# Kernel tuning notes

Hardware: AMD Instinct MI355X
Metric: run time of the kernel (lower is better)

Reference implementation:

```python
import jax, jax.numpy as jnp
import numpy as np

N = 50000   # nodes
E = 800000  # edges (avg degree 16)
F_IN = 128
H = 128
L = 4
LN_EPS = 1e-5


def setup_inputs() -> dict:
    key = jax.random.key(0)
    ks = jax.random.split(key, 4)
    x = jax.random.normal(ks[0], (N, F_IN), dtype=jnp.float32)
    edge_index = jax.random.randint(ks[1], (2, E), 0, N)
    conv_w = jax.random.normal(ks[2], (L, F_IN, H), dtype=jnp.float32) * 0.05
    conv_b = jnp.zeros((L, H), dtype=jnp.float32)
    ln_g = jnp.ones((L, H), dtype=jnp.float32)
    ln_b = jnp.zeros((L, H), dtype=jnp.float32)
    head_w = jax.random.normal(ks[3], (H, 1), dtype=jnp.float32) * 0.05
    head_b = jnp.zeros((1,), dtype=jnp.float32)
    return {"x": x, "edge_index": edge_index, "conv_w": conv_w, "conv_b": conv_b,
            "ln_g": ln_g, "ln_b": ln_b, "head_w": head_w, "head_b": head_b}


def _layer_norm(h, g, b):
    mu = jnp.mean(h, axis=-1, keepdims=True)
    var = jnp.mean(jnp.square(h - mu), axis=-1, keepdims=True)
    return (h - mu) * jax.lax.rsqrt(var + LN_EPS) * g + b


def _gcn_conv(h, W, b, src, dst, inv_sqrt_deg, inv_deg):
    # PyG GCNConv: self-loops + symmetric normalization D^-1/2 (A+I) D^-1/2, then bias.
    hw = h @ W  # (N, H)
    norm = inv_sqrt_deg[src] * inv_sqrt_deg[dst]  # (E,)
    msg = hw[src] * norm[:, None]  # gather + edgewise scale
    agg = jax.ops.segment_sum(msg, dst, num_segments=N)  # scatter-add
    agg = agg + hw * inv_deg[:, None]  # self-loop term (norm = 1/deg)
    return agg + b


def reference(x, edge_index, conv_w, conv_b, ln_g, ln_b, head_w, head_b):
    src, dst = edge_index[0], edge_index[1]
    # degree on target nodes, including self-loop
    deg = jax.ops.segment_sum(jnp.ones((E,), x.dtype), dst, num_segments=N) + 1.0
    inv_sqrt_deg = jax.lax.rsqrt(deg)
    inv_deg = 1.0 / deg
    h = x
    for i in range(L):
        h = _gcn_conv(h, conv_w[i], conv_b[i], src, dst, inv_sqrt_deg, inv_deg)
        h = _layer_norm(h, ln_g[i], ln_b[i])
        if i != L - 1:
            h = jax.nn.gelu(h, approximate=False)
            # dropout is identity in eval mode
    scores = (h @ head_w + head_b).squeeze(-1)  # (N,)
    return scores, h
```

## Files before the change

kernel.cpp:

```cpp
#include <hip/hip_runtime.h>
#include <math.h>

#define N_NODES 50000
#define N_EDGES 800000
#define HDIM 128
#define NLAYERS 4
#define LN_EPS 1e-5f

typedef __attribute__((ext_vector_type(8))) short short8;
typedef __attribute__((ext_vector_type(4))) float floatx4;

__device__ __forceinline__ ushort f2bf(float x) {
    unsigned b = __float_as_uint(x);
    unsigned r = b + 0x7fffu + ((b >> 16) & 1u);
    return (ushort)(r >> 16);
}
__device__ __forceinline__ float2 bf2f2(unsigned u) {
    return make_float2(__uint_as_float(u << 16), __uint_as_float(u & 0xffff0000u));
}


__global__ void deg_count_kernel(const int* __restrict__ dst, int* __restrict__ degcnt) {
    int e = blockIdx.x * blockDim.x + threadIdx.x;
    if (e < N_EDGES) atomicAdd(&degcnt[dst[e]], 1);
}

__global__ void scan1_kernel(const int* __restrict__ degcnt, int* __restrict__ partial,
                             int* __restrict__ blocksum) {
    __shared__ int buf[256];
    int tid = threadIdx.x;
    int i = blockIdx.x * 256 + tid;
    int v = (i < N_NODES) ? degcnt[i] : 0;
    buf[tid] = v;
    __syncthreads();
    for (int off = 1; off < 256; off <<= 1) {
        int t = (tid >= off) ? buf[tid - off] : 0;
        __syncthreads();
        buf[tid] += t;
        __syncthreads();
    }
    if (i < N_NODES) partial[i] = buf[tid] - v;
    if (tid == 255) blocksum[blockIdx.x] = buf[255];
}

__global__ void scan2_kernel(int* __restrict__ blocksum, int nblk) {
    __shared__ int buf[256];
    int tid = threadIdx.x;
    int v = (tid < nblk) ? blocksum[tid] : 0;
    buf[tid] = v;
    __syncthreads();
    for (int off = 1; off < 256; off <<= 1) {
        int t = (tid >= off) ? buf[tid - off] : 0;
        __syncthreads();
        buf[tid] += t;
        __syncthreads();
    }
    if (tid < nblk) blocksum[tid] = buf[tid] - v;
}

__global__ void scan3_kernel(const int* __restrict__ degcnt, const int* __restrict__ partial,
                             const int* __restrict__ blocksum, int* __restrict__ offs,
                             int* __restrict__ cursor, float* __restrict__ isd,
                             float* __restrict__ ind) {
    int i = blockIdx.x * blockDim.x + threadIdx.x;
    if (i < N_NODES) {
        int o = partial[i] + blocksum[i >> 8];
        offs[i] = o;
        cursor[i] = o;
        float d = (float)degcnt[i] + 1.0f;
        isd[i] = rsqrtf(d);
        ind[i] = 1.0f / d;
        if (i == 0) offs[N_NODES] = N_EDGES;
    }
}

__global__ void fill_kernel(const int* __restrict__ src, const int* __restrict__ dst,
                            const float* __restrict__ isd, int* __restrict__ cursor,
                            int* __restrict__ csr_src, float* __restrict__ csr_w) {
    int e = blockIdx.x * blockDim.x + threadIdx.x;
    if (e < N_EDGES) {
        int s = src[e], d = dst[e];
        int p = atomicAdd(&cursor[d], 1);
        csr_src[p] = s;
        csr_w[p] = isd[s] * isd[d];
    }
}

__global__ __launch_bounds__(256) void bprep_kernel(const float* __restrict__ W,
                                                    ushort* __restrict__ bfrag) {
    int idx = blockIdx.x * 256 + threadIdx.x;
    if (idx >= NLAYERS * 4 * 8 * 64) return;
    int lane = idx & 63;
    int t = (idx >> 6) & 7;
    int s = (idx >> 9) & 3;
    int l = idx >> 11;
    int n = t * 16 + (lane & 15);
    int kb = s * 32 + (lane >> 4) * 8;
    const float* Wl = W + (size_t)l * HDIM * HDIM;
    union { uint4 q; ushort u[8]; } o;
#pragma unroll
    for (int j = 0; j < 8; ++j) o.u[j] = f2bf(Wl[(size_t)(kb + j) * HDIM + n]);
    *(uint4*)&bfrag[(size_t)idx * 8] = o.q;
}

template <bool A_FP32>
__global__ __launch_bounds__(256) void gemm_mfma_kernel(const void* __restrict__ Av,
                                                        const ushort* __restrict__ bfrag,
                                                        ushort* __restrict__ out) {
    int wave = threadIdx.x >> 6, lane = threadIdx.x & 63;
    int quad = lane >> 4, mrow = lane & 15;
    int rowBase = blockIdx.x * 64 + wave * 16;
    int arow = rowBase + mrow;
    bool aok = arow < N_NODES;

    floatx4 acc[8];
#pragma unroll
    for (int t = 0; t < 8; ++t) acc[t] = (floatx4)0.f;

#pragma unroll
    for (int s = 0; s < 4; ++s) {
        union { short8 v; ushort u[8]; } af;
        if (A_FP32) {
            const float* A = (const float*)Av;
            if (aok) {
                const float* p = &A[(size_t)arow * HDIM + s * 32 + quad * 8];
#pragma unroll
                for (int j = 0; j < 8; ++j) af.u[j] = f2bf(p[j]);
            } else {
#pragma unroll
                for (int j = 0; j < 8; ++j) af.u[j] = 0;
            }
        } else {
            const ushort* A = (const ushort*)Av;
            if (aok) {
                af.v = *(const short8*)&A[(size_t)arow * HDIM + s * 32 + quad * 8];
            } else {
#pragma unroll
                for (int j = 0; j < 8; ++j) af.u[j] = 0;
            }
        }
#pragma unroll
        for (int t = 0; t < 8; ++t) {
            short8 bf = *(const short8*)&bfrag[(size_t)(((s * 8 + t) * 64) + lane) * 8];
            acc[t] = __builtin_amdgcn_mfma_f32_16x16x32_bf16(af.v, bf, acc[t], 0, 0, 0);
        }
    }
#pragma unroll
    for (int t = 0; t < 8; ++t) {
#pragma unroll
        for (int r = 0; r < 4; ++r) {
            int row = rowBase + quad * 4 + r;
            if (row < N_NODES) out[(size_t)row * HDIM + t * 16 + mrow] = f2bf(acc[t][r]);
        }
    }
}

__global__ __launch_bounds__(256) void agg_ln_kernel(
    const unsigned* __restrict__ hwu, const int* __restrict__ offs,
    const int* __restrict__ csr_src, const float* __restrict__ csr_w,
    const float* __restrict__ ind, const float* __restrict__ conv_b,
    const float* __restrict__ ln_g, const float* __restrict__ ln_b,
    unsigned* __restrict__ hout_bf, float* __restrict__ hout_f32,
    const float* __restrict__ head_w, const float* __restrict__ head_b,
    float* __restrict__ scores, int final_layer) {
    int wave = threadIdx.x >> 6;
    int lane = threadIdx.x & 63;
    int n = blockIdx.x * 4 + wave;
    if (n >= N_NODES) return;
    int c = lane * 2;

    float2 hv = bf2f2(hwu[(size_t)n * 64 + lane]);
    float idn = ind[n];
    float2 cb = *(const float2*)&conv_b[c];
    float ax = fmaf(hv.x, idn, cb.x);
    float ay = fmaf(hv.y, idn, cb.y);

    int rs = offs[n], re = offs[n + 1];
    for (int base = rs; base < re; base += 64) {
        int m = re - base;
        if (m > 64) m = 64;
        int sj = 0;
        float wj = 0.f;
        if (lane < m) { sj = csr_src[base + lane]; wj = csr_w[base + lane]; }
        int j = 0;
        for (; j + 4 <= m; j += 4) {
            int s0 = __shfl(sj, j + 0), s1 = __shfl(sj, j + 1);
            int s2 = __shfl(sj, j + 2), s3 = __shfl(sj, j + 3);
            float w0 = __shfl(wj, j + 0), w1 = __shfl(wj, j + 1);
            float w2 = __shfl(wj, j + 2), w3 = __shfl(wj, j + 3);
            unsigned u0 = hwu[(size_t)s0 * 64 + lane];
            unsigned u1 = hwu[(size_t)s1 * 64 + lane];
            unsigned u2 = hwu[(size_t)s2 * 64 + lane];
            unsigned u3 = hwu[(size_t)s3 * 64 + lane];
            float2 v0 = bf2f2(u0), v1 = bf2f2(u1), v2 = bf2f2(u2), v3 = bf2f2(u3);
            ax = fmaf(v0.x, w0, ax); ay = fmaf(v0.y, w0, ay);
            ax = fmaf(v1.x, w1, ax); ay = fmaf(v1.y, w1, ay);
            ax = fmaf(v2.x, w2, ax); ay = fmaf(v2.y, w2, ay);
            ax = fmaf(v3.x, w3, ax); ay = fmaf(v3.y, w3, ay);
        }
        for (; j < m; ++j) {
            int s = __shfl(sj, j);
            float w = __shfl(wj, j);
            float2 v = bf2f2(hwu[(size_t)s * 64 + lane]);
            ax = fmaf(v.x, w, ax);
            ay = fmaf(v.y, w, ay);
        }
    }

    float sum = ax + ay;
#pragma unroll
    for (int o = 32; o; o >>= 1) sum += __shfl_xor(sum, o);
    float mu = sum * (1.0f / HDIM);
    float dx = ax - mu, dy = ay - mu;
    float vs = dx * dx + dy * dy;
#pragma unroll
    for (int o = 32; o; o >>= 1) vs += __shfl_xor(vs, o);
    float rstd = rsqrtf(vs * (1.0f / HDIM) + LN_EPS);
    float2 g = *(const float2*)&ln_g[c];
    float2 b = *(const float2*)&ln_b[c];
    float yx = fmaf(dx * rstd, g.x, b.x);
    float yy = fmaf(dy * rstd, g.y, b.y);

    if (!final_layer) {
        yx = 0.5f * yx * (1.0f + erff(yx * 0.70710678118654752f));
        yy = 0.5f * yy * (1.0f + erff(yy * 0.70710678118654752f));
        hout_bf[(size_t)n * 64 + lane] = (unsigned)f2bf(yx) | ((unsigned)f2bf(yy) << 16);
    } else {
        *(float2*)&hout_f32[(size_t)n * HDIM + c] = make_float2(yx, yy);
        float2 hwv = *(const float2*)&head_w[c];
        float p = yx * hwv.x + yy * hwv.y;
#pragma unroll
        for (int o = 32; o; o >>= 1) p += __shfl_xor(p, o);
        if (lane == 0) scores[n] = p + head_b[0];
    }
}


extern "C" void kernel_launch(void* const* d_in, const int* in_sizes, int n_in,
                              void* d_out, int out_size, void* d_ws, size_t ws_size,
                              hipStream_t stream) {
    const float* x      = (const float*)d_in[0];
    const int*   eidx   = (const int*)d_in[1];
    const float* conv_w = (const float*)d_in[2];
    const float* conv_b = (const float*)d_in[3];
    const float* ln_g   = (const float*)d_in[4];
    const float* ln_b   = (const float*)d_in[5];
    const float* head_w = (const float*)d_in[6];
    const float* head_b = (const float*)d_in[7];
    float* out = (float*)d_out;

    const int* src = eidx;
    const int* dst = eidx + N_EDGES;

    char* ws = (char*)d_ws;
    size_t o = 0;
    auto alloc = [&](size_t elems) {
        void* p = ws + o * 4;
        o += (elems + 15) & ~(size_t)15;
        return p;
    };
    int*      degcnt   = (int*)alloc(N_NODES);
    float*    isd      = (float*)alloc(N_NODES);
    float*    ind      = (float*)alloc(N_NODES);
    int*      offs     = (int*)alloc(N_NODES + 1);
    int*      cursor   = (int*)alloc(N_NODES);
    int*      partial  = (int*)alloc(N_NODES);
    int*      blocksum = (int*)alloc(256);
    int*      csr_src  = (int*)alloc(N_EDGES);
    float*    csr_w    = (float*)alloc(N_EDGES);
    ushort*   bfrag    = (ushort*)alloc(NLAYERS * 4 * 8 * 64 * 8 / 2);
    unsigned* hw       = (unsigned*)alloc((size_t)N_NODES * 64);
    unsigned* hbuf     = (unsigned*)alloc((size_t)N_NODES * 64);

    hipMemsetAsync(degcnt, 0, N_NODES * sizeof(int), stream);
    deg_count_kernel<<<(N_EDGES + 255) / 256, 256, 0, stream>>>(dst, degcnt);
    int nblk = (N_NODES + 255) / 256;
    scan1_kernel<<<nblk, 256, 0, stream>>>(degcnt, partial, blocksum);
    scan2_kernel<<<1, 256, 0, stream>>>(blocksum, nblk);
    scan3_kernel<<<nblk, 256, 0, stream>>>(degcnt, partial, blocksum, offs, cursor, isd, ind);
    fill_kernel<<<(N_EDGES + 255) / 256, 256, 0, stream>>>(src, dst, isd, cursor, csr_src, csr_w);
    bprep_kernel<<<(NLAYERS * 4 * 8 * 64 + 255) / 256, 256, 0, stream>>>(conv_w, bfrag);

    const void* hin = (const void*)x;
    for (int l = 0; l < NLAYERS; ++l) {
        const ushort* bl = bfrag + (size_t)l * 4 * 8 * 64 * 8;
        if (l == 0)
            gemm_mfma_kernel<true><<<(N_NODES + 63) / 64, 256, 0, stream>>>(hin, bl, (ushort*)hw);
        else
            gemm_mfma_kernel<false><<<(N_NODES + 63) / 64, 256, 0, stream>>>(hin, bl, (ushort*)hw);
        int fin = (l == NLAYERS - 1) ? 1 : 0;
        agg_ln_kernel<<<(N_NODES + 3) / 4, 256, 0, stream>>>(
            hw, offs, csr_src, csr_w, ind,
            conv_b + (size_t)l * HDIM, ln_g + (size_t)l * HDIM, ln_b + (size_t)l * HDIM,
            hbuf, out + N_NODES, head_w, head_b, out, fin);
        hin = (const void*)hbuf;
    }
}
```

Measured before the change: 403.6 us.

## Compact CSR to 16-bit indices, atomic wave-level allocation, compute edge weights on the fly

Replaces the three-kernel prefix scan with a single kernel that does a wave-level scan and claims each wave's offset range with one atomic, so segments are no longer in node order. The CSR stores only 16-bit source indices, which is valid because there are fewer than 65536 nodes, and drops the per-edge float weight. The aggregation kernel looks up isd[src] per edge and applies isd[dst] once per node. The gather loop is unrolled to 8, with padded lanes carrying weight zero. This cuts CSR memory traffic and kernel launches, at the cost of an extra isd gather per edge and wasted padded loads for low-degree nodes.

```diff
diff --git a/kernel.cpp b/kernel.cpp
--- a/kernel.cpp
+++ b/kernel.cpp
@@ -25,64 +25,40 @@
     if (e < N_EDGES) atomicAdd(&degcnt[dst[e]], 1);
 }
 
-__global__ void scan1_kernel(const int* __restrict__ degcnt, int* __restrict__ partial,
-                             int* __restrict__ blocksum) {
-    __shared__ int buf[256];
-    int tid = threadIdx.x;
-    int i = blockIdx.x * 256 + tid;
-    int v = (i < N_NODES) ? degcnt[i] : 0;
-    buf[tid] = v;
-    __syncthreads();
-    for (int off = 1; off < 256; off <<= 1) {
-        int t = (tid >= off) ? buf[tid - off] : 0;
-        __syncthreads();
-        buf[tid] += t;
-        __syncthreads();
-    }
-    if (i < N_NODES) partial[i] = buf[tid] - v;
-    if (tid == 255) blocksum[blockIdx.x] = buf[255];
-}
-
-__global__ void scan2_kernel(int* __restrict__ blocksum, int nblk) {
-    __shared__ int buf[256];
-    int tid = threadIdx.x;
-    int v = (tid < nblk) ? blocksum[tid] : 0;
-    buf[tid] = v;
-    __syncthreads();
-    for (int off = 1; off < 256; off <<= 1) {
-        int t = (tid >= off) ? buf[tid - off] : 0;
-        __syncthreads();
-        buf[tid] += t;
-        __syncthreads();
-    }
-    if (tid < nblk) blocksum[tid] = buf[tid] - v;
-}
-
-__global__ void scan3_kernel(const int* __restrict__ degcnt, const int* __restrict__ partial,
-                             const int* __restrict__ blocksum, int* __restrict__ offs,
-                             int* __restrict__ cursor, float* __restrict__ isd,
-                             float* __restrict__ ind) {
-    int i = blockIdx.x * blockDim.x + threadIdx.x;
+__global__ __launch_bounds__(256) void alloc_kernel(
+    const int* __restrict__ degcnt, int* __restrict__ counter,
+    int* __restrict__ start, int* __restrict__ cursor,
+    float* __restrict__ isd, float* __restrict__ ind) {
+    int i = blockIdx.x * 256 + threadIdx.x;
+    int lane = threadIdx.x & 63;
+    int deg = (i < N_NODES) ? degcnt[i] : 0;
+    int v = deg;
+#pragma unroll
+    for (int off = 1; off < 64; off <<= 1) {
+        int t = __shfl_up(v, off);
+        if (lane >= off) v += t;
+    }
+    int total = __shfl(v, 63);
+    int base = 0;
+    if (lane == 63) base = atomicAdd(counter, total);
+    base = __shfl(base, 63);
     if (i < N_NODES) {
-        int o = partial[i] + blocksum[i >> 8];
-        offs[i] = o;
-        cursor[i] = o;
-        float d = (float)degcnt[i] + 1.0f;
+        int st = base + v - deg;
+        start[i] = st;
+        cursor[i] = st;
+        float d = (float)deg + 1.0f;
         isd[i] = rsqrtf(d);
         ind[i] = 1.0f / d;
-        if (i == 0) offs[N_NODES] = N_EDGES;
     }
 }
 
 __global__ void fill_kernel(const int* __restrict__ src, const int* __restrict__ dst,
-                            const float* __restrict__ isd, int* __restrict__ cursor,
-                            int* __restrict__ csr_src, float* __restrict__ csr_w) {
+                            int* __restrict__ cursor, ushort* __restrict__ csr16) {
     int e = blockIdx.x * blockDim.x + threadIdx.x;
     if (e < N_EDGES) {
         int s = src[e], d = dst[e];
         int p = atomicAdd(&cursor[d], 1);
-        csr_src[p] = s;
-        csr_w[p] = isd[s] * isd[d];
+        csr16[p] = (ushort)s;
     }
 }
 
@@ -156,13 +132,14 @@
 }
 
 __global__ __launch_bounds__(256) void agg_ln_kernel(
-    const unsigned* __restrict__ hwu, const int* __restrict__ offs,
-    const int* __restrict__ csr_src, const float* __restrict__ csr_w,
-    const float* __restrict__ ind, const float* __restrict__ conv_b,
-    const float* __restrict__ ln_g, const float* __restrict__ ln_b,
-    unsigned* __restrict__ hout_bf, float* __restrict__ hout_f32,
-    const float* __restrict__ head_w, const float* __restrict__ head_b,
-    float* __restrict__ scores, int final_layer) {
+    const unsigned* __restrict__ hwu, const int* __restrict__ start,
+    const int* __restrict__ degcnt, const ushort* __restrict__ csr16,
+    const float* __restrict__ isd, const float* __restrict__ ind,
+    const float* __restrict__ conv_b, const float* __restrict__ ln_g,
+    const float* __restrict__ ln_b, unsigned* __restrict__ hout_bf,
+    float* __restrict__ hout_f32, const float* __restrict__ head_w,
+    const float* __restrict__ head_b, float* __restrict__ scores,
+    int final_layer) {
     int wave = threadIdx.x >> 6;
     int lane = threadIdx.x & 63;
     int n = blockIdx.x * 4 + wave;
@@ -170,42 +147,53 @@
     int c = lane * 2;
 
     float2 hv = bf2f2(hwu[(size_t)n * 64 + lane]);
-    float idn = ind[n];
-    float2 cb = *(const float2*)&conv_b[c];
-    float ax = fmaf(hv.x, idn, cb.x);
-    float ay = fmaf(hv.y, idn, cb.y);
-
-    int rs = offs[n], re = offs[n + 1];
-    for (int base = rs; base < re; base += 64) {
-        int m = re - base;
+    float isd_n = isd[n];
+    float ind_n = ind[n];
+    int rs = start[n];
+    int deg = degcnt[n];
+
+    float ex = 0.f, ey = 0.f;
+    for (int b0 = 0; b0 < deg; b0 += 64) {
+        int m = deg - b0;
         if (m > 64) m = 64;
         int sj = 0;
         float wj = 0.f;
-        if (lane < m) { sj = csr_src[base + lane]; wj = csr_w[base + lane]; }
-        int j = 0;
-        for (; j + 4 <= m; j += 4) {
+        if (lane < m) {
+            sj = (int)csr16[rs + b0 + lane];
+            wj = isd[sj];
+        }
+        for (int j = 0; j < m; j += 8) {
             int s0 = __shfl(sj, j + 0), s1 = __shfl(sj, j + 1);
             int s2 = __shfl(sj, j + 2), s3 = __shfl(sj, j + 3);
+            int s4 = __shfl(sj, j + 4), s5 = __shfl(sj, j + 5);
+            int s6 = __shfl(sj, j + 6), s7 = __shfl(sj, j + 7);
             float w0 = __shfl(wj, j + 0), w1 = __shfl(wj, j + 1);
             float w2 = __shfl(wj, j + 2), w3 = __shfl(wj, j + 3);
+            float w4 = __shfl(wj, j + 4), w5 = __shfl(wj, j + 5);
+            float w6 = __shfl(wj, j + 6), w7 = __shfl(wj, j + 7);
             unsigned u0 = hwu[(size_t)s0 * 64 + lane];
             unsigned u1 = hwu[(size_t)s1 * 64 + lane];
             unsigned u2 = hwu[(size_t)s2 * 64 + lane];
             unsigned u3 = hwu[(size_t)s3 * 64 + lane];
+            unsigned u4 = hwu[(size_t)s4 * 64 + lane];
+            unsigned u5 = hwu[(size_t)s5 * 64 + lane];
+            unsigned u6 = hwu[(size_t)s6 * 64 + lane];
+            unsigned u7 = hwu[(size_t)s7 * 64 + lane];
             float2 v0 = bf2f2(u0), v1 = bf2f2(u1), v2 = bf2f2(u2), v3 = bf2f2(u3);
-            ax = fmaf(v0.x, w0, ax); ay = fmaf(v0.y, w0, ay);
-            ax = fmaf(v1.x, w1, ax); ay = fmaf(v1.y, w1, ay);
-            ax = fmaf(v2.x, w2, ax); ay = fmaf(v2.y, w2, ay);
-            ax = fmaf(v3.x, w3, ax); ay = fmaf(v3.y, w3, ay);
-        }
-        for (; j < m; ++j) {
-            int s = __shfl(sj, j);
-            float w = __shfl(wj, j);
-            float2 v = bf2f2(hwu[(size_t)s * 64 + lane]);
-            ax = fmaf(v.x, w, ax);
-            ay = fmaf(v.y, w, ay);
-        }
-    }
+            float2 v4 = bf2f2(u4), v5 = bf2f2(u5), v6 = bf2f2(u6), v7 = bf2f2(u7);
+            ex = fmaf(v0.x, w0, ex); ey = fmaf(v0.y, w0, ey);
+            ex = fmaf(v1.x, w1, ex); ey = fmaf(v1.y, w1, ey);
+            ex = fmaf(v2.x, w2, ex); ey = fmaf(v2.y, w2, ey);
+            ex = fmaf(v3.x, w3, ex); ey = fmaf(v3.y, w3, ey);
+            ex = fmaf(v4.x, w4, ex); ey = fmaf(v4.y, w4, ey);
+            ex = fmaf(v5.x, w5, ex); ey = fmaf(v5.y, w5, ey);
+            ex = fmaf(v6.x, w6, ex); ey = fmaf(v6.y, w6, ey);
+            ex = fmaf(v7.x, w7, ex); ey = fmaf(v7.y, w7, ey);
+        }
+    }
+    float2 cb = *(const float2*)&conv_b[c];
+    float ax = fmaf(ex, isd_n, fmaf(hv.x, ind_n, cb.x));
+    float ay = fmaf(ey, isd_n, fmaf(hv.y, ind_n, cb.y));
 
     float sum = ax + ay;
 #pragma unroll
@@ -260,25 +248,21 @@
         return p;
     };
     int*      degcnt   = (int*)alloc(N_NODES);
+    int*      counter  = (int*)alloc(16);
     float*    isd      = (float*)alloc(N_NODES);
     float*    ind      = (float*)alloc(N_NODES);
-    int*      offs     = (int*)alloc(N_NODES + 1);
+    int*      start    = (int*)alloc(N_NODES);
     int*      cursor   = (int*)alloc(N_NODES);
-    int*      partial  = (int*)alloc(N_NODES);
-    int*      blocksum = (int*)alloc(256);
-    int*      csr_src  = (int*)alloc(N_EDGES);
-    float*    csr_w    = (float*)alloc(N_EDGES);
+    ushort*   csr16    = (ushort*)alloc(N_EDGES / 2);
     ushort*   bfrag    = (ushort*)alloc(NLAYERS * 4 * 8 * 64 * 8 / 2);
     unsigned* hw       = (unsigned*)alloc((size_t)N_NODES * 64);
     unsigned* hbuf     = (unsigned*)alloc((size_t)N_NODES * 64);
 
-    hipMemsetAsync(degcnt, 0, N_NODES * sizeof(int), stream);
+    hipMemsetAsync(degcnt, 0, (N_NODES + 16) * sizeof(int), stream);
     deg_count_kernel<<<(N_EDGES + 255) / 256, 256, 0, stream>>>(dst, degcnt);
     int nblk = (N_NODES + 255) / 256;
-    scan1_kernel<<<nblk, 256, 0, stream>>>(degcnt, partial, blocksum);
-    scan2_kernel<<<1, 256, 0, stream>>>(blocksum, nblk);
-    scan3_kernel<<<nblk, 256, 0, stream>>>(degcnt, partial, blocksum, offs, cursor, isd, ind);
-    fill_kernel<<<(N_EDGES + 255) / 256, 256, 0, stream>>>(src, dst, isd, cursor, csr_src, csr_w);
+    alloc_kernel<<<nblk, 256, 0, stream>>>(degcnt, counter, start, cursor, isd, ind);
+    fill_kernel<<<(N_EDGES + 255) / 256, 256, 0, stream>>>(src, dst, cursor, csr16);
     bprep_kernel<<<(NLAYERS * 4 * 8 * 64 + 255) / 256, 256, 0, stream>>>(conv_w, bfrag);
 
     const void* hin = (const void*)x;
@@ -290,7 +274,7 @@
             gemm_mfma_kernel<false><<<(N_NODES + 63) / 64, 256, 0, stream>>>(hin, bl, (ushort*)hw);
         int fin = (l == NLAYERS - 1) ? 1 : 0;
         agg_ln_kernel<<<(N_NODES + 3) / 4, 256, 0, stream>>>(
-            hw, offs, csr_src, csr_w, ind,
+            hw, start, degcnt, csr16, isd, ind,
             conv_b + (size_t)l * HDIM, ln_g + (size_t)l * HDIM, ln_b + (size_t)l * HDIM,
             hbuf, out + N_NODES, head_w, head_b, out, fin);
         hin = (const void*)hbuf;
```

Measured after the change: 370.0 us. -8.3%, faster.
